# Kernel optimization log

Measured on AMD Instinct MI355X. Metric: run time of the kernel, lower is better.

The kernel has to match this reference:

```python
import jax, jax.numpy as jnp
import numpy as np
import math

N_HEADS = 16
KV_HEADS = 4
HEAD_DIM = 128
ROPE_BASE = 1000000.0


def _make_rope(seq_len, dim, base=ROPE_BASE):
    inv_freq = 1.0 / (base ** (np.arange(0, dim, 2, dtype=np.float32) / dim))
    t = np.arange(seq_len, dtype=np.float32)
    freqs = np.outer(t, inv_freq)                     # [S, dim/2]
    emb = np.concatenate([freqs, freqs], axis=-1)     # [S, dim]
    return jnp.asarray(np.cos(emb)), jnp.asarray(np.sin(emb))


def setup_inputs() -> dict:
    key = jax.random.key(0)
    ks = jax.random.split(key, 6)
    B, S, H = 2, 2048, 2048
    kv_dim = KV_HEADS * HEAD_DIM
    s = 1.0 / math.sqrt(H)
    x = jax.random.normal(ks[0], (B, S, H), jnp.float32)
    wq = jax.random.normal(ks[1], (H, H), jnp.float32) * s
    wk = jax.random.normal(ks[2], (kv_dim, H), jnp.float32) * s
    wv = jax.random.normal(ks[3], (kv_dim, H), jnp.float32) * s
    wo = jax.random.normal(ks[4], (H, H), jnp.float32) * s
    bq = jnp.zeros((H,), jnp.float32)
    bk = jnp.zeros((kv_dim,), jnp.float32)
    bv = jnp.zeros((kv_dim,), jnp.float32)
    bo = jnp.zeros((H,), jnp.float32)
    cos, sin = _make_rope(S, HEAD_DIM)
    return {"x": x, "wq": wq, "bq": bq, "wk": wk, "bk": bk,
            "wv": wv, "bv": bv, "wo": wo, "bo": bo, "cos": cos, "sin": sin}


def _rotate_half(t):
    half = t.shape[-1] // 2
    return jnp.concatenate([-t[..., half:], t[..., :half]], axis=-1)


def reference(x, wq, bq, wk, bk, wv, bv, wo, bo, cos, sin):
    B, S, H = x.shape
    hd, nh, kvh = HEAD_DIM, N_HEADS, KV_HEADS
    rep = nh // kvh

    q = (x @ wq.T + bq).reshape(B, S, nh, hd)
    k = (x @ wk.T + bk).reshape(B, S, kvh, hd)
    v = (x @ wv.T + bv).reshape(B, S, kvh, hd)

    # RoPE (rotate-half), cos/sin: [S, hd] -> broadcast over batch and heads
    c = cos[None, :, None, :]
    s_ = sin[None, :, None, :]
    q = q * c + _rotate_half(q) * s_
    k = k * c + _rotate_half(k) * s_

    # GQA: expand KV heads by rep
    k = jnp.repeat(k, rep, axis=2)   # [B, S, nh, hd]
    v = jnp.repeat(v, rep, axis=2)

    q = q.transpose(0, 2, 1, 3)      # [B, nh, S, hd]
    k = k.transpose(0, 2, 1, 3)
    v = v.transpose(0, 2, 1, 3)

    score = jnp.einsum('bhqd,bhkd->bhqk', q, k) / math.sqrt(hd)
    causal = jnp.triu(jnp.full((S, S), -jnp.inf, jnp.float32), k=1)
    score = score + causal
    attn = jax.nn.softmax(score.astype(jnp.float32), axis=-1).astype(q.dtype)

    out = jnp.einsum('bhqk,bhkd->bhqd', attn, v)   # [B, nh, S, hd]
    out = out.transpose(0, 2, 1, 3).reshape(B, S, nh * hd)
    return out @ wo.T + bo
```

## Files before the change

### kernel.cpp

```cpp
#include <hip/hip_runtime.h>

typedef unsigned short u16;
typedef __bf16 bf16x8 __attribute__((ext_vector_type(8)));
typedef float  f32x4  __attribute__((ext_vector_type(4)));

#define SEQ 2048

__device__ __forceinline__ float bf2f(u16 u) {
    union { unsigned int i; float f; } c;
    c.i = ((unsigned int)u) << 16;
    return c.f;
}
__device__ __forceinline__ u16 f2bf(float f) {
    union { float f; unsigned int i; } c;
    c.f = f;
    unsigned int u = c.i;
    u += 0x7FFFu + ((u >> 16) & 1u);
    return (u16)(u >> 16);
}

__device__ __forceinline__ void gl_lds16(const u16* g, u16* l) {
    __builtin_amdgcn_global_load_lds(
        (const __attribute__((address_space(1))) unsigned int*)(g),
        (__attribute__((address_space(3))) unsigned int*)(l), 16, 0, 0);
}

__device__ __forceinline__ void cvt4(const float* s, u16* d) {
    float4 v = *(const float4*)s;
    ushort4 o;
    o.x = f2bf(v.x); o.y = f2bf(v.y); o.z = f2bf(v.z); o.w = f2bf(v.w);
    *(ushort4*)d = o;
}

__global__ void prep(const float* __restrict__ x,
                     const float* __restrict__ wq, const float* __restrict__ wk,
                     const float* __restrict__ wv,
                     const float* __restrict__ bq, const float* __restrict__ bk,
                     const float* __restrict__ bv,
                     u16* __restrict__ xb, u16* __restrict__ wqkvb,
                     float* __restrict__ biasb)
{
    const int E0 = 2097152;
    const int E1 = E0 + 1048576;
    const int E2 = E1 + 262144;
    const int E3 = E2 + 262144;
    const int E4 = E3 + 768;
    int i = blockIdx.x * blockDim.x + threadIdx.x;
    int stride = gridDim.x * blockDim.x;
    for (; i < E4; i += stride) {
        if (i < E0)      cvt4(x  + (size_t)i * 4,        xb    + (size_t)i * 4);
        else if (i < E1) cvt4(wq + (size_t)(i - E0) * 4, wqkvb + (size_t)(i - E0) * 4);
        else if (i < E2) cvt4(wk + (size_t)(i - E1) * 4, wqkvb + 4194304 + (size_t)(i - E1) * 4);
        else if (i < E3) cvt4(wv + (size_t)(i - E2) * 4, wqkvb + 5242880 + (size_t)(i - E2) * 4);
        else {
            int j = i - E3;
            const float* src = (j < 512) ? (bq + j * 4)
                             : (j < 640) ? (bk + (j - 512) * 4)
                                         : (bv + (j - 640) * 4);
            *(float4*)&biasb[j * 4] = *(const float4*)src;
        }
    }
}

__global__ void cvt_f32_bf16(const float* __restrict__ in, u16* __restrict__ out, int n4) {
    int i = blockIdx.x * blockDim.x + threadIdx.x;
    int stride = gridDim.x * blockDim.x;
    for (; i < n4; i += stride) cvt4(in + (size_t)i * 4, out + (size_t)i * 4);
}

template<int MODE>
__global__ __launch_bounds__(256) void gemm_bt(
    const u16* __restrict__ A, const u16* __restrict__ B,
    const float* __restrict__ bias, float* __restrict__ C,
    u16* __restrict__ qb, u16* __restrict__ kb, u16* __restrict__ vt,
    int M, int N, int K)
{
    __shared__ __align__(16) u16 lA[128 * 32];
    __shared__ __align__(16) u16 lB[128 * 32];
    const int tid   = threadIdx.x;
    const int lane  = tid & 63;
    const int wave  = tid >> 6;
    const int waveM = (wave >> 1) * 64;
    const int waveN = (wave & 1) * 64;
    const int bm = blockIdx.x * 128;
    const int bn = blockIdx.y * 128;
    const int lrow = lane & 15;
    const int koff = (lane >> 4) * 8;

    f32x4 acc[4][4] = {};

    for (int k0 = 0; k0 < K; k0 += 32) {
        __syncthreads();
#pragma unroll
        for (int p = 0; p < 2; ++p) {
            int idx = p * 256 + tid;
            int row = idx >> 2;
            int ch  = idx & 3;
            gl_lds16(&A[(size_t)(bm + row) * K + k0 + ch * 8], &lA[(p * 256 + wave * 64) * 8]);
            gl_lds16(&B[(size_t)(bn + row) * K + k0 + ch * 8], &lB[(p * 256 + wave * 64) * 8]);
        }
        __syncthreads();

        bf16x8 af[4], bfr[4];
#pragma unroll
        for (int i = 0; i < 4; ++i)
            af[i] = *(const bf16x8*)&lA[(waveM + i * 16 + lrow) * 32 + koff];
#pragma unroll
        for (int j = 0; j < 4; ++j)
            bfr[j] = *(const bf16x8*)&lB[(waveN + j * 16 + lrow) * 32 + koff];
#pragma unroll
        for (int i = 0; i < 4; ++i)
#pragma unroll
            for (int j = 0; j < 4; ++j)
                acc[i][j] = __builtin_amdgcn_mfma_f32_16x16x32_bf16(
                    af[i], bfr[j], acc[i][j], 0, 0, 0);
    }

    const int r4 = (lane >> 4) * 4;
    const int cn = lane & 15;
#pragma unroll
    for (int i = 0; i < 4; ++i) {
#pragma unroll
        for (int j = 0; j < 4; ++j) {
            int row0 = bm + waveM + i * 16 + r4;
            int col  = bn + waveN + j * 16 + cn;
            float bc = bias[col];
#pragma unroll
            for (int r = 0; r < 4; ++r) {
                float val = acc[i][j][r] + bc;
                if (MODE == 0) {
                    C[(size_t)(row0 + r) * N + col] = val;
                } else {
                    int row = row0 + r;
                    int b = row >> 11;
                    int s = row & 2047;
                    int d = col & 127;
                    u16 o = f2bf(val);
                    if (col < 2048) {
                        int h = col >> 7;
                        qb[(((size_t)(b * 16 + h) * SEQ) + s) * 128 + d] = o;
                    } else if (col < 2560) {
                        int h = (col - 2048) >> 7;
                        kb[(((size_t)(b * 4 + h) * SEQ) + s) * 128 + d] = o;
                    } else {
                        int h = (col - 2560) >> 7;
                        vt[(((size_t)(b * 4 + h) * 128) + d) * SEQ + s] = o;
                    }
                }
            }
        }
    }
}

__global__ void rope_inplace(u16* __restrict__ qb, u16* __restrict__ kb,
                             const float* __restrict__ cosb, const float* __restrict__ sinb)
{
    const int n = (65536 + 16384) * 64;
    int i = blockIdx.x * blockDim.x + threadIdx.x;
    if (i >= n) return;
    int d0  = i & 63;
    int row = i >> 6;
    u16* base;
    if (row < 65536) base = qb + (size_t)row * 128;
    else             base = kb + (size_t)(row - 65536) * 128;
    int s = row & (SEQ - 1);
    float c  = cosb[s * 128 + d0];
    float sn = sinb[s * 128 + d0];
    float a0 = bf2f(base[d0]);
    float a1 = bf2f(base[d0 + 64]);
    base[d0]      = f2bf(a0 * c - a1 * sn);
    base[d0 + 64] = f2bf(a1 * c + a0 * sn);
}

__global__ __launch_bounds__(256, 2) void attn_mfma(
    const u16* __restrict__ qb, const u16* __restrict__ kb,
    const u16* __restrict__ vt, u16* __restrict__ ob)
{
    __shared__ __align__(16) u16 Ks[4][128][32];
    __shared__ __align__(16) u16 Vts[4][128][32];
    __shared__ __align__(16) u16 Ph[4][16][64];

    const int pair = blockIdx.x;
    const int qA   = pair, qB = 31 - pair;
    const int h    = blockIdx.y;
    const int b    = blockIdx.z;
    const int kvh  = h >> 2;
    const int tid  = threadIdx.x;
    const int lane = tid & 63;
    const int w    = tid >> 6;
    const int c16  = lane & 15;
    const int quad = lane >> 4;
    const float qscale = 0.08838834764831845f * 1.4426950408889634f;

    const u16* kbase  = kb + ((size_t)(b * 4 + kvh) * SEQ) * 128;
    const u16* vtbase = vt + ((size_t)(b * 4 + kvh) * 128) * SEQ;

    bf16x8 qfA[4], qfB[4];
    {
        const u16* qpA = qb + (((size_t)(b * 16 + h)) * SEQ + qA * 64 + w * 16 + c16) * 128;
        const u16* qpB = qb + (((size_t)(b * 16 + h)) * SEQ + qB * 64 + w * 16 + c16) * 128;
#pragma unroll
        for (int kk = 0; kk < 4; ++kk) {
            bf16x8 ta = *(const bf16x8*)(qpA + kk * 32 + quad * 8);
            bf16x8 tb = *(const bf16x8*)(qpB + kk * 32 + quad * 8);
#pragma unroll
            for (int e = 0; e < 8; ++e) {
                ta[e] = (__bf16)((float)ta[e] * qscale);
                tb[e] = (__bf16)((float)tb[e] * qscale);
            }
            qfA[kk] = ta; qfB[kk] = tb;
        }
    }

    int ksrc[8], vsrc[8];
#pragma unroll
    for (int it = 0; it < 8; ++it) {
        int o  = (it * 4 + w) * 1024 + lane * 16;
        int kk = o >> 13;
        int r  = (o >> 6) & 127;
        int c  = (o >> 4) & 3;
        ksrc[it] = r * 128 + kk * 32 + c * 8;
        vsrc[it] = r * SEQ + kk * 32 + c * 8;
    }

    const int nA = (qA + 2) >> 1;
    const int nB = (qB + 2) >> 1;
    const int rowLA = qA * 64 + w * 16 + quad * 4;
    const int rowLB = qB * 64 + w * 16 + quad * 4;

    f32x4 oA[8] = {}, oB[8] = {};
    float lA[4] = {}, lB[4] = {};

    u16* KsF  = &Ks[0][0][0];
    u16* VtsF = &Vts[0][0][0];

    for (int kt = 0; kt < nB; ++kt) {
        __syncthreads();
        const u16* kg = kbase + (size_t)kt * (128 * 128);
        const u16* vg = vtbase + kt * 128;
#pragma unroll
        for (int it = 0; it < 8; ++it) {
            gl_lds16(kg + ksrc[it], &KsF[(it * 4 + w) * 512]);
            gl_lds16(vg + vsrc[it], &VtsF[(it * 4 + w) * 512]);
        }
        __syncthreads();

        const bool doA = kt < nA;
        f32x4 sA[8] = {}, sB[8] = {};
        if (doA) {
#pragma unroll
            for (int kk = 0; kk < 4; ++kk)
#pragma unroll
                for (int j = 0; j < 8; ++j) {
                    bf16x8 kf = *(const bf16x8*)&Ks[kk][j * 16 + c16][quad * 8];
                    sA[j] = __builtin_amdgcn_mfma_f32_16x16x32_bf16(qfA[kk], kf, sA[j], 0, 0, 0);
                    sB[j] = __builtin_amdgcn_mfma_f32_16x16x32_bf16(qfB[kk], kf, sB[j], 0, 0, 0);
                }
        } else {
#pragma unroll
            for (int kk = 0; kk < 4; ++kk)
#pragma unroll
                for (int j = 0; j < 8; ++j) {
                    bf16x8 kf = *(const bf16x8*)&Ks[kk][j * 16 + c16][quad * 8];
                    sB[j] = __builtin_amdgcn_mfma_f32_16x16x32_bf16(qfB[kk], kf, sB[j], 0, 0, 0);
                }
        }

        if (doA && kt == nA - 1) {
#pragma unroll
            for (int j = 0; j < 8; ++j)
#pragma unroll
                for (int rr = 0; rr < 4; ++rr)
                    if (kt * 128 + j * 16 + c16 > rowLA + rr) sA[j][rr] = -1e30f;
        }
        if (kt == nB - 1) {
#pragma unroll
            for (int j = 0; j < 8; ++j)
#pragma unroll
                for (int rr = 0; rr < 4; ++rr)
                    if (kt * 128 + j * 16 + c16 > rowLB + rr) sB[j][rr] = -1e30f;
        }

#pragma unroll
        for (int hf = 0; hf < 2; ++hf) {
            bf16x8 paA[2], paB[2];
            if (doA) {
#pragma unroll
                for (int jj = 0; jj < 4; ++jj) {
                    int j = hf * 4 + jj;
#pragma unroll
                    for (int rr = 0; rr < 4; ++rr) {
                        float p = __builtin_amdgcn_exp2f(sA[j][rr]);
                        lA[rr] += p;
                        int row = quad * 4 + rr;
                        Ph[w][row][(((jj * 2 + (c16 >> 3)) + row) & 7) * 8 + (c16 & 7)] = f2bf(p);
                    }
                }
#pragma unroll
                for (int k2 = 0; k2 < 2; ++k2)
                    paA[k2] = *(const bf16x8*)&Ph[w][c16][(((k2 * 4 + quad) + c16) & 7) * 8];
            }
#pragma unroll
            for (int jj = 0; jj < 4; ++jj) {
                int j = hf * 4 + jj;
#pragma unroll
                for (int rr = 0; rr < 4; ++rr) {
                    float p = __builtin_amdgcn_exp2f(sB[j][rr]);
                    lB[rr] += p;
                    int row = quad * 4 + rr;
                    Ph[w][row][(((jj * 2 + (c16 >> 3)) + row) & 7) * 8 + (c16 & 7)] = f2bf(p);
                }
            }
#pragma unroll
            for (int k2 = 0; k2 < 2; ++k2)
                paB[k2] = *(const bf16x8*)&Ph[w][c16][(((k2 * 4 + quad) + c16) & 7) * 8];

            if (doA) {
#pragma unroll
                for (int k2 = 0; k2 < 2; ++k2)
#pragma unroll
                    for (int nt = 0; nt < 8; ++nt) {
                        bf16x8 vf = *(const bf16x8*)&Vts[hf * 2 + k2][nt * 16 + c16][quad * 8];
                        oA[nt] = __builtin_amdgcn_mfma_f32_16x16x32_bf16(paA[k2], vf, oA[nt], 0, 0, 0);
                        oB[nt] = __builtin_amdgcn_mfma_f32_16x16x32_bf16(paB[k2], vf, oB[nt], 0, 0, 0);
                    }
            } else {
#pragma unroll
                for (int k2 = 0; k2 < 2; ++k2)
#pragma unroll
                    for (int nt = 0; nt < 8; ++nt) {
                        bf16x8 vf = *(const bf16x8*)&Vts[hf * 2 + k2][nt * 16 + c16][quad * 8];
                        oB[nt] = __builtin_amdgcn_mfma_f32_16x16x32_bf16(paB[k2], vf, oB[nt], 0, 0, 0);
                    }
            }
        }
    }

    float liA[4], liB[4];
#pragma unroll
    for (int rr = 0; rr < 4; ++rr) {
        float la = lA[rr], lb = lB[rr];
        la += __shfl_xor(la, 1); lb += __shfl_xor(lb, 1);
        la += __shfl_xor(la, 2); lb += __shfl_xor(lb, 2);
        la += __shfl_xor(la, 4); lb += __shfl_xor(lb, 4);
        la += __shfl_xor(la, 8); lb += __shfl_xor(lb, 8);
        liA[rr] = 1.0f / la;     liB[rr] = 1.0f / lb;
    }
    const size_t rowGA = (size_t)b * SEQ + rowLA;
    const size_t rowGB = (size_t)b * SEQ + rowLB;
#pragma unroll
    for (int nt = 0; nt < 8; ++nt)
#pragma unroll
        for (int rr = 0; rr < 4; ++rr) {
            ob[(rowGA + rr) * 2048 + h * 128 + nt * 16 + c16] = f2bf(oA[nt][rr] * liA[rr]);
            ob[(rowGB + rr) * 2048 + h * 128 + nt * 16 + c16] = f2bf(oB[nt][rr] * liB[rr]);
        }
}

extern "C" void kernel_launch(void* const* d_in, const int* in_sizes, int n_in,
                              void* d_out, int out_size, void* d_ws, size_t ws_size,
                              hipStream_t stream) {
    const float* x    = (const float*)d_in[0];
    const float* wq   = (const float*)d_in[1];
    const float* bq   = (const float*)d_in[2];
    const float* wk   = (const float*)d_in[3];
    const float* bk   = (const float*)d_in[4];
    const float* wv   = (const float*)d_in[5];
    const float* bv   = (const float*)d_in[6];
    const float* wo   = (const float*)d_in[7];
    const float* bo   = (const float*)d_in[8];
    const float* cosb = (const float*)d_in[9];
    const float* sinb = (const float*)d_in[10];
    float* out = (float*)d_out;

    char* ws = (char*)d_ws;
    const size_t OFF_WQKV = 0;
    const size_t OFF_BIAS = 12582912;
    const size_t OFF_QB   = 12599296;
    const size_t OFF_KB   = 29376512;
    const size_t OFF_VT   = 33570816;
    const size_t OFF_XB   = 37765120;

    u16*   wqkvb = (u16*)(ws + OFF_WQKV);
    u16*   wob   = (u16*)(ws + OFF_WQKV);
    float* biasb = (float*)(ws + OFF_BIAS);
    u16*   qb2   = (u16*)(ws + OFF_QB);
    u16*   kb2   = (u16*)(ws + OFF_KB);
    u16*   vt2   = (u16*)(ws + OFF_VT);
    u16*   xb    = (u16*)(ws + OFF_XB);
    u16*   attnb = (u16*)(ws + OFF_XB);

    prep<<<4096, 256, 0, stream>>>(x, wq, wk, wv, bq, bk, bv, xb, wqkvb, biasb);

    gemm_bt<1><<<dim3(32, 24), 256, 0, stream>>>(xb, wqkvb, biasb, nullptr,
                                                 qb2, kb2, vt2, 4096, 3072, 2048);

    cvt_f32_bf16<<<4096, 256, 0, stream>>>(wo, wob, 1048576);

    rope_inplace<<<((65536 + 16384) * 64) / 256, 256, 0, stream>>>(qb2, kb2, cosb, sinb);

    attn_mfma<<<dim3(16, 16, 2), 256, 0, stream>>>(qb2, kb2, vt2, attnb);

    gemm_bt<0><<<dim3(32, 16), 256, 0, stream>>>(attnb, wob, bo, out,
                                                 nullptr, nullptr, nullptr, 4096, 2048, 2048);
}
```

Baseline: 346.1 us.

## Double-buffer K/V tiles with async LDS prefetch and halve KV tile size

Shrinks the attention KV tile from 128 to 64 keys and double-buffers K and V^T in shared memory. The next tile's global-to-LDS loads are issued before computing on the current one, with explicit vmcnt waits and raw barriers. MFMA sections are wrapped in s_setprio. This hides global load latency behind compute, at the cost of twice as many loop iterations and barriers. The smaller tile also trims wasted work on the diagonal causal tile.

```diff
diff --git a/kernel.cpp b/kernel.cpp
--- a/kernel.cpp
+++ b/kernel.cpp
@@ -176,8 +176,8 @@
     const u16* __restrict__ qb, const u16* __restrict__ kb,
     const u16* __restrict__ vt, u16* __restrict__ ob)
 {
-    __shared__ __align__(16) u16 Ks[4][128][32];
-    __shared__ __align__(16) u16 Vts[4][128][32];
+    __shared__ __align__(16) u16 Ks[2][4][64][32];
+    __shared__ __align__(16) u16 Vts[2][2][128][32];
     __shared__ __align__(16) u16 Ph[4][16][64];
 
     const int pair = blockIdx.x;
@@ -212,47 +212,68 @@
         }
     }
 
-    int ksrc[8], vsrc[8];
-#pragma unroll
-    for (int it = 0; it < 8; ++it) {
+    int ksrc[4], vsrc[4];
+#pragma unroll
+    for (int it = 0; it < 4; ++it) {
         int o  = (it * 4 + w) * 1024 + lane * 16;
-        int kk = o >> 13;
-        int r  = (o >> 6) & 127;
+        int kk = o >> 12;
+        int r  = (o >> 6) & 63;
         int c  = (o >> 4) & 3;
         ksrc[it] = r * 128 + kk * 32 + c * 8;
-        vsrc[it] = r * SEQ + kk * 32 + c * 8;
-    }
-
-    const int nA = (qA + 2) >> 1;
-    const int nB = (qB + 2) >> 1;
+        int p2 = o >> 13;
+        int d  = (o >> 6) & 127;
+        vsrc[it] = d * SEQ + p2 * 32 + c * 8;
+    }
+
+    const int nB = qB + 1;
     const int rowLA = qA * 64 + w * 16 + quad * 4;
     const int rowLB = qB * 64 + w * 16 + quad * 4;
 
     f32x4 oA[8] = {}, oB[8] = {};
     float lA[4] = {}, lB[4] = {};
 
-    u16* KsF  = &Ks[0][0][0];
-    u16* VtsF = &Vts[0][0][0];
+    u16* KsF  = &Ks[0][0][0][0];
+    u16* VtsF = &Vts[0][0][0][0];
+
+    asm volatile("s_waitcnt vmcnt(0)" ::: "memory");
+
+#pragma unroll
+    for (int it = 0; it < 4; ++it) {
+        gl_lds16(kbase  + ksrc[it], KsF  + (it * 4 + w) * 512);
+        gl_lds16(vtbase + vsrc[it], VtsF + (it * 4 + w) * 512);
+    }
 
     for (int kt = 0; kt < nB; ++kt) {
-        __syncthreads();
-        const u16* kg = kbase + (size_t)kt * (128 * 128);
-        const u16* vg = vtbase + kt * 128;
-#pragma unroll
-        for (int it = 0; it < 8; ++it) {
-            gl_lds16(kg + ksrc[it], &KsF[(it * 4 + w) * 512]);
-            gl_lds16(vg + vsrc[it], &VtsF[(it * 4 + w) * 512]);
-        }
-        __syncthreads();
-
-        const bool doA = kt < nA;
-        f32x4 sA[8] = {}, sB[8] = {};
+        const int cur = kt & 1;
+        if (kt + 1 < nB) {
+            const u16* kg = kbase  + (size_t)(kt + 1) * (64 * 128);
+            const u16* vg = vtbase + (kt + 1) * 64;
+            u16* kd = KsF  + ((kt + 1) & 1) * (4 * 64 * 32);
+            u16* vd = VtsF + ((kt + 1) & 1) * (2 * 128 * 32);
+#pragma unroll
+            for (int it = 0; it < 4; ++it) {
+                gl_lds16(kg + ksrc[it], kd + (it * 4 + w) * 512);
+                gl_lds16(vg + vsrc[it], vd + (it * 4 + w) * 512);
+            }
+            asm volatile("s_waitcnt vmcnt(8)" ::: "memory");
+        } else {
+            asm volatile("s_waitcnt vmcnt(0)" ::: "memory");
+        }
+        __builtin_amdgcn_s_barrier();
+        asm volatile("" ::: "memory");
+
+        const u16* Kb = KsF  + cur * (4 * 64 * 32);
+        const u16* Vb = VtsF + cur * (2 * 128 * 32);
+        const bool doA = kt <= qA;
+
+        f32x4 sA[4] = {}, sB[4] = {};
+        __builtin_amdgcn_s_setprio(1);
         if (doA) {
 #pragma unroll
             for (int kk = 0; kk < 4; ++kk)
 #pragma unroll
-                for (int j = 0; j < 8; ++j) {
-                    bf16x8 kf = *(const bf16x8*)&Ks[kk][j * 16 + c16][quad * 8];
+                for (int j = 0; j < 4; ++j) {
+                    bf16x8 kf = *(const bf16x8*)(Kb + (size_t)(kk * 64 + j * 16 + c16) * 32 + quad * 8);
                     sA[j] = __builtin_amdgcn_mfma_f32_16x16x32_bf16(qfA[kk], kf, sA[j], 0, 0, 0);
                     sB[j] = __builtin_amdgcn_mfma_f32_16x16x32_bf16(qfB[kk], kf, sB[j], 0, 0, 0);
                 }
@@ -260,80 +281,79 @@
 #pragma unroll
             for (int kk = 0; kk < 4; ++kk)
 #pragma unroll
-                for (int j = 0; j < 8; ++j) {
-                    bf16x8 kf = *(const bf16x8*)&Ks[kk][j * 16 + c16][quad * 8];
+                for (int j = 0; j < 4; ++j) {
+                    bf16x8 kf = *(const bf16x8*)(Kb + (size_t)(kk * 64 + j * 16 + c16) * 32 + quad * 8);
                     sB[j] = __builtin_amdgcn_mfma_f32_16x16x32_bf16(qfB[kk], kf, sB[j], 0, 0, 0);
                 }
         }
-
-        if (doA && kt == nA - 1) {
-#pragma unroll
-            for (int j = 0; j < 8; ++j)
+        __builtin_amdgcn_s_setprio(0);
+
+        if (doA && kt == qA) {
+#pragma unroll
+            for (int j = 0; j < 4; ++j)
 #pragma unroll
                 for (int rr = 0; rr < 4; ++rr)
-                    if (kt * 128 + j * 16 + c16 > rowLA + rr) sA[j][rr] = -1e30f;
-        }
-        if (kt == nB - 1) {
-#pragma unroll
-            for (int j = 0; j < 8; ++j)
+                    if (kt * 64 + j * 16 + c16 > rowLA + rr) sA[j][rr] = -1e30f;
+        }
+        if (kt == qB) {
+#pragma unroll
+            for (int j = 0; j < 4; ++j)
 #pragma unroll
                 for (int rr = 0; rr < 4; ++rr)
-                    if (kt * 128 + j * 16 + c16 > rowLB + rr) sB[j][rr] = -1e30f;
-        }
-
-#pragma unroll
-        for (int hf = 0; hf < 2; ++hf) {
-            bf16x8 paA[2], paB[2];
-            if (doA) {
-#pragma unroll
-                for (int jj = 0; jj < 4; ++jj) {
-                    int j = hf * 4 + jj;
-#pragma unroll
-                    for (int rr = 0; rr < 4; ++rr) {
-                        float p = __builtin_amdgcn_exp2f(sA[j][rr]);
-                        lA[rr] += p;
-                        int row = quad * 4 + rr;
-                        Ph[w][row][(((jj * 2 + (c16 >> 3)) + row) & 7) * 8 + (c16 & 7)] = f2bf(p);
-                    }
-                }
-#pragma unroll
-                for (int k2 = 0; k2 < 2; ++k2)
-                    paA[k2] = *(const bf16x8*)&Ph[w][c16][(((k2 * 4 + quad) + c16) & 7) * 8];
-            }
-#pragma unroll
-            for (int jj = 0; jj < 4; ++jj) {
-                int j = hf * 4 + jj;
+                    if (kt * 64 + j * 16 + c16 > rowLB + rr) sB[j][rr] = -1e30f;
+        }
+
+        bf16x8 paA[2], paB[2];
+        if (doA) {
+#pragma unroll
+            for (int jj = 0; jj < 4; ++jj)
 #pragma unroll
                 for (int rr = 0; rr < 4; ++rr) {
-                    float p = __builtin_amdgcn_exp2f(sB[j][rr]);
-                    lB[rr] += p;
+                    float p = __builtin_amdgcn_exp2f(sA[jj][rr]);
+                    lA[rr] += p;
                     int row = quad * 4 + rr;
                     Ph[w][row][(((jj * 2 + (c16 >> 3)) + row) & 7) * 8 + (c16 & 7)] = f2bf(p);
                 }
+#pragma unroll
+            for (int k2 = 0; k2 < 2; ++k2)
+                paA[k2] = *(const bf16x8*)&Ph[w][c16][(((k2 * 4 + quad) + c16) & 7) * 8];
+        }
+#pragma unroll
+        for (int jj = 0; jj < 4; ++jj)
+#pragma unroll
+            for (int rr = 0; rr < 4; ++rr) {
+                float p = __builtin_amdgcn_exp2f(sB[jj][rr]);
+                lB[rr] += p;
+                int row = quad * 4 + rr;
+                Ph[w][row][(((jj * 2 + (c16 >> 3)) + row) & 7) * 8 + (c16 & 7)] = f2bf(p);
             }
 #pragma unroll
+        for (int k2 = 0; k2 < 2; ++k2)
+            paB[k2] = *(const bf16x8*)&Ph[w][c16][(((k2 * 4 + quad) + c16) & 7) * 8];
+
+        __builtin_amdgcn_s_setprio(1);
+        if (doA) {
+#pragma unroll
             for (int k2 = 0; k2 < 2; ++k2)
-                paB[k2] = *(const bf16x8*)&Ph[w][c16][(((k2 * 4 + quad) + c16) & 7) * 8];
-
-            if (doA) {
-#pragma unroll
-                for (int k2 = 0; k2 < 2; ++k2)
-#pragma unroll
-                    for (int nt = 0; nt < 8; ++nt) {
-                        bf16x8 vf = *(const bf16x8*)&Vts[hf * 2 + k2][nt * 16 + c16][quad * 8];
-                        oA[nt] = __builtin_amdgcn_mfma_f32_16x16x32_bf16(paA[k2], vf, oA[nt], 0, 0, 0);
-                        oB[nt] = __builtin_amdgcn_mfma_f32_16x16x32_bf16(paB[k2], vf, oB[nt], 0, 0, 0);
-                    }
-            } else {
-#pragma unroll
-                for (int k2 = 0; k2 < 2; ++k2)
-#pragma unroll
-                    for (int nt = 0; nt < 8; ++nt) {
-                        bf16x8 vf = *(const bf16x8*)&Vts[hf * 2 + k2][nt * 16 + c16][quad * 8];
-                        oB[nt] = __builtin_amdgcn_mfma_f32_16x16x32_bf16(paB[k2], vf, oB[nt], 0, 0, 0);
-                    }
-            }
-        }
+#pragma unroll
+                for (int nt = 0; nt < 8; ++nt) {
+                    bf16x8 vf = *(const bf16x8*)(Vb + (size_t)(k2 * 128 + nt * 16 + c16) * 32 + quad * 8);
+                    oA[nt] = __builtin_amdgcn_mfma_f32_16x16x32_bf16(paA[k2], vf, oA[nt], 0, 0, 0);
+                    oB[nt] = __builtin_amdgcn_mfma_f32_16x16x32_bf16(paB[k2], vf, oB[nt], 0, 0, 0);
+                }
+        } else {
+#pragma unroll
+            for (int k2 = 0; k2 < 2; ++k2)
+#pragma unroll
+                for (int nt = 0; nt < 8; ++nt) {
+                    bf16x8 vf = *(const bf16x8*)(Vb + (size_t)(k2 * 128 + nt * 16 + c16) * 32 + quad * 8);
+                    oB[nt] = __builtin_amdgcn_mfma_f32_16x16x32_bf16(paB[k2], vf, oB[nt], 0, 0, 0);
+                }
+        }
+        __builtin_amdgcn_s_setprio(0);
+
+        asm volatile("" ::: "memory");
+        __builtin_amdgcn_s_barrier();
     }
 
     float liA[4], liB[4];
```

Measured after the change: 377.9 us. +9.2%, slower.
